# Kernel tuning notes

Measured on AMD Instinct MI355X. Metric: run time of the kernel, lower is better.

The kernel has to match this reference:

```python
import jax, jax.numpy as jnp
import numpy as np

DIM = 4096
NUM_EXPERTS = 8
TOP_K = 2
TOKENS = 8192  # batch 2 * seq 4096


def setup_inputs() -> dict:
    key = jax.random.key(0)
    k1, k2 = jax.random.split(key)
    x = jax.random.normal(k1, (TOKENS, DIM), dtype=jnp.float32)
    W = jax.random.normal(k2, (NUM_EXPERTS, DIM), dtype=jnp.float32) * 0.02  # router weight, trunc-normal-ish
    return {"x": x, "W": W}


def reference(x, W):
    # Routing: linear -> top-k -> softmax over the k selected scores (fp32) -> cast back
    expert_scores = jnp.einsum("td,ed->te", x, W)                       # [T, E]
    top_scores, selected = jax.lax.top_k(expert_scores, TOP_K)          # [T, K], [T, K]
    top_scores = jax.nn.softmax(top_scores.astype(jnp.float32), axis=-1).astype(x.dtype)

    flat_expert_indices = selected.reshape(-1)                           # [T*K]
    # torch.histc(bins=E, min=0, max=E) on integer expert ids == bincount
    num_tokens_per_expert = jnp.bincount(flat_expert_indices, length=NUM_EXPERTS)

    # Stable argsort groups tokens by destination expert, preserving token order within an expert
    sorted_indices = jnp.argsort(flat_expert_indices, stable=True)       # [T*K]
    scatter_indices = sorted_indices // TOP_K                            # original token id per slot
    x_gathered = x[scatter_indices]                                      # [T*K, D]
    scores_sorted = top_scores.reshape(-1)[sorted_indices]               # [T*K]
    return x_gathered, num_tokens_per_expert, scatter_indices, scores_sorted
```

## Files before the change

kernel.cpp:

```cpp
#include <hip/hip_runtime.h>
#include <hip/hip_bf16.h>
#include <cstdint>

#define TOKENS 8192
#define DIM 4096
#define D4 (DIM / 4)
#define NEXP 8
#define TOPK 2
#define SLOTS (TOKENS * TOPK)
#define NCHUNK (SLOTS / 64)

#define OUT_X 0
#define OUT_CNT ((size_t)TOKENS * TOPK * DIM)
#define OUT_SCAT (OUT_CNT + NEXP)
#define OUT_SCORE (OUT_SCAT + SLOTS)

__global__ __launch_bounds__(256) void k_score(const float* __restrict__ x,
                                               const float* __restrict__ W,
                                               int* __restrict__ eid,
                                               float* __restrict__ prob)
{
    const int wave = threadIdx.x >> 6;
    const int lane = threadIdx.x & 63;
    const int tok0 = (blockIdx.x * 4 + wave) * 8;

    const float4* x4 = reinterpret_cast<const float4*>(x);
    const float4* W4 = reinterpret_cast<const float4*>(W);

    float acc[8][NEXP];
#pragma unroll
    for (int t = 0; t < 8; ++t)
#pragma unroll
        for (int e = 0; e < NEXP; ++e) acc[t][e] = 0.f;

    for (int i = 0; i < 16; ++i) {
        const int d4 = lane + 64 * i;
        float4 w[NEXP];
#pragma unroll
        for (int e = 0; e < NEXP; ++e) w[e] = W4[e * D4 + d4];
#pragma unroll
        for (int t = 0; t < 8; ++t) {
            const float4 xv = x4[(size_t)(tok0 + t) * D4 + d4];
#pragma unroll
            for (int e = 0; e < NEXP; ++e) {
                acc[t][e] = fmaf(xv.x, w[e].x, acc[t][e]);
                acc[t][e] = fmaf(xv.y, w[e].y, acc[t][e]);
                acc[t][e] = fmaf(xv.z, w[e].z, acc[t][e]);
                acc[t][e] = fmaf(xv.w, w[e].w, acc[t][e]);
            }
        }
    }

#pragma unroll
    for (int t = 0; t < 8; ++t)
#pragma unroll
        for (int e = 0; e < NEXP; ++e) {
            float v = acc[t][e];
#pragma unroll
            for (int off = 32; off >= 1; off >>= 1) v += __shfl_xor(v, off);
            acc[t][e] = v;
        }

#pragma unroll
    for (int t = 0; t < 8; ++t) {
        int i0 = 0;
        float m0 = acc[t][0];
#pragma unroll
        for (int e = 1; e < NEXP; ++e)
            if (acc[t][e] > m0) { m0 = acc[t][e]; i0 = e; }
        int i1 = -1;
        float m1 = -INFINITY;
#pragma unroll
        for (int e = 0; e < NEXP; ++e)
            if (e != i0 && acc[t][e] > m1) { m1 = acc[t][e]; i1 = e; }
        const float z = __expf(m1 - m0);
        const float inv = 1.0f / (1.0f + z);
        if (lane == t) {
            const int s2 = (tok0 + t) * 2;
            eid[s2] = i0;
            eid[s2 + 1] = i1;
            prob[s2] = inv;
            prob[s2 + 1] = z * inv;
        }
    }
}

__global__ __launch_bounds__(1024) void k_sort(const int* __restrict__ eid,
                                               const float* __restrict__ prob,
                                               int* __restrict__ dstpos,
                                               float* __restrict__ out)
{
    __shared__ int hist[NCHUNK][NEXP];
    const int tid = threadIdx.x;
    const int wave = tid >> 6;
    const int lane = tid & 63;

    for (int c = wave; c < NCHUNK; c += 16) {
        const int s = c * 64 + lane;
        const int e = eid[s];
#pragma unroll
        for (int q = 0; q < NEXP; ++q) {
            const unsigned long long m = __ballot(e == q);
            if (lane == q) hist[c][q] = __popcll(m);
        }
    }
    __syncthreads();

    if (wave == 0) {
        int run[NEXP];
#pragma unroll
        for (int q = 0; q < NEXP; ++q) run[q] = 0;

        for (int r = 0; r < 4; ++r) {
            const int c = r * 64 + lane;
#pragma unroll
            for (int q = 0; q < NEXP; ++q) {
                const int v = hist[c][q];
                int incl = v;
#pragma unroll
                for (int off = 1; off <= 32; off <<= 1) {
                    const int n = __shfl_up(incl, off);
                    if (lane >= off) incl += n;
                }
                hist[c][q] = run[q] + incl - v;
                run[q] += __shfl(incl, 63);
            }
        }
        int eoff[NEXP];
        int a = 0;
#pragma unroll
        for (int q = 0; q < NEXP; ++q) { eoff[q] = a; a += run[q]; }
        for (int r = 0; r < 4; ++r) {
            const int c = r * 64 + lane;
#pragma unroll
            for (int q = 0; q < NEXP; ++q) hist[c][q] += eoff[q];
        }
        if (lane == 0) {
#pragma unroll
            for (int q = 0; q < NEXP; ++q) out[OUT_CNT + q] = (float)run[q];
        }
    }
    __syncthreads();

    for (int c = wave; c < NCHUNK; c += 16) {
        const int s = c * 64 + lane;
        const int e = eid[s];
        const unsigned long long lt = (1ull << lane) - 1ull;
        int rank = 0;
#pragma unroll
        for (int q = 0; q < NEXP; ++q) {
            const unsigned long long m = __ballot(e == q);
            if (e == q) rank = __popcll(m & lt);
        }
        const int p = hist[c][e] + rank;
        dstpos[s] = p;
        out[OUT_SCAT + p] = (float)(s >> 1);
        out[OUT_SCORE + p] = prob[s];
    }
}

__global__ __launch_bounds__(256) void k_gather(const float* __restrict__ x,
                                                const int* __restrict__ dstpos,
                                                float* __restrict__ out)
{
    const int t = blockIdx.x;
    const int p0 = dstpos[t * 2];
    const int p1 = dstpos[t * 2 + 1];
    const float4* x4 = reinterpret_cast<const float4*>(x) + (size_t)t * D4;
    float4* o4 = reinterpret_cast<float4*>(out);
#pragma unroll
    for (int i = 0; i < 4; ++i) {
        const int idx = threadIdx.x + 256 * i;
        const float4 v = x4[idx];
        o4[(size_t)p0 * D4 + idx] = v;
        o4[(size_t)p1 * D4 + idx] = v;
    }
}

extern "C" void kernel_launch(void* const* d_in, const int* in_sizes, int n_in,
                              void* d_out, int out_size, void* d_ws, size_t ws_size,
                              hipStream_t stream)
{
    const float* x = (const float*)d_in[0];
    const float* W = (const float*)d_in[1];
    float* out = (float*)d_out;

    int* eid = (int*)d_ws;
    float* prob = (float*)((char*)d_ws + 64 * 1024);
    int* dstpos = (int*)((char*)d_ws + 128 * 1024);

    k_score<<<TOKENS / 32, 256, 0, stream>>>(x, W, eid, prob);
    k_sort<<<1, 1024, 0, stream>>>(eid, prob, dstpos, out);
    k_gather<<<TOKENS, 256, 0, stream>>>(x, dstpos, out);
}
```

Baseline: 444.9 us.

## Split single-block sort into multi-block hist/scan/pos kernels, retile scoring, nontemporal gather stores

Replaces the single 1024-thread sort kernel with three kernels: a per-chunk histogram across 256 blocks, a one-wave scan, and a per-chunk position/scatter pass across 256 blocks. This spreads the serial sort across the GPU. The scoring kernel drops from 8 to 4 tokens per wave and reorders its loops to load x first, which doubles the block count and lowers register pressure. The gather kernel now uses nontemporal stores for the large output so it does not pollute cache, at the cost of two extra kernel launches.

```diff
diff --git a/kernel.cpp b/kernel.cpp
--- a/kernel.cpp
+++ b/kernel.cpp
@@ -10,10 +10,11 @@
 #define SLOTS (TOKENS * TOPK)
 #define NCHUNK (SLOTS / 64)
 
-#define OUT_X 0
 #define OUT_CNT ((size_t)TOKENS * TOPK * DIM)
 #define OUT_SCAT (OUT_CNT + NEXP)
 #define OUT_SCORE (OUT_SCAT + SLOTS)
+
+typedef float vfloat4 __attribute__((ext_vector_type(4)));
 
 __global__ __launch_bounds__(256) void k_score(const float* __restrict__ x,
                                                const float* __restrict__ W,
@@ -22,37 +23,37 @@
 {
     const int wave = threadIdx.x >> 6;
     const int lane = threadIdx.x & 63;
-    const int tok0 = (blockIdx.x * 4 + wave) * 8;
+    const int tok0 = (blockIdx.x * 4 + wave) * 4;
 
     const float4* x4 = reinterpret_cast<const float4*>(x);
     const float4* W4 = reinterpret_cast<const float4*>(W);
 
-    float acc[8][NEXP];
-#pragma unroll
-    for (int t = 0; t < 8; ++t)
+    float acc[4][NEXP];
+#pragma unroll
+    for (int t = 0; t < 4; ++t)
 #pragma unroll
         for (int e = 0; e < NEXP; ++e) acc[t][e] = 0.f;
 
     for (int i = 0; i < 16; ++i) {
         const int d4 = lane + 64 * i;
-        float4 w[NEXP];
-#pragma unroll
-        for (int e = 0; e < NEXP; ++e) w[e] = W4[e * D4 + d4];
-#pragma unroll
-        for (int t = 0; t < 8; ++t) {
-            const float4 xv = x4[(size_t)(tok0 + t) * D4 + d4];
-#pragma unroll
-            for (int e = 0; e < NEXP; ++e) {
-                acc[t][e] = fmaf(xv.x, w[e].x, acc[t][e]);
-                acc[t][e] = fmaf(xv.y, w[e].y, acc[t][e]);
-                acc[t][e] = fmaf(xv.z, w[e].z, acc[t][e]);
-                acc[t][e] = fmaf(xv.w, w[e].w, acc[t][e]);
+        float4 xv[4];
+#pragma unroll
+        for (int t = 0; t < 4; ++t) xv[t] = x4[(size_t)(tok0 + t) * D4 + d4];
+#pragma unroll
+        for (int e = 0; e < NEXP; ++e) {
+            const float4 w = W4[e * D4 + d4];
+#pragma unroll
+            for (int t = 0; t < 4; ++t) {
+                acc[t][e] = fmaf(xv[t].x, w.x, acc[t][e]);
+                acc[t][e] = fmaf(xv[t].y, w.y, acc[t][e]);
+                acc[t][e] = fmaf(xv[t].z, w.z, acc[t][e]);
+                acc[t][e] = fmaf(xv[t].w, w.w, acc[t][e]);
             }
         }
     }
 
 #pragma unroll
-    for (int t = 0; t < 8; ++t)
+    for (int t = 0; t < 4; ++t)
 #pragma unroll
         for (int e = 0; e < NEXP; ++e) {
             float v = acc[t][e];
@@ -62,7 +63,7 @@
         }
 
 #pragma unroll
-    for (int t = 0; t < 8; ++t) {
+    for (int t = 0; t < 4; ++t) {
         int i0 = 0;
         float m0 = acc[t][0];
 #pragma unroll
@@ -85,78 +86,79 @@
     }
 }
 
-__global__ __launch_bounds__(1024) void k_sort(const int* __restrict__ eid,
-                                               const float* __restrict__ prob,
-                                               int* __restrict__ dstpos,
-                                               float* __restrict__ out)
-{
-    __shared__ int hist[NCHUNK][NEXP];
-    const int tid = threadIdx.x;
-    const int wave = tid >> 6;
-    const int lane = tid & 63;
-
-    for (int c = wave; c < NCHUNK; c += 16) {
-        const int s = c * 64 + lane;
-        const int e = eid[s];
+__global__ __launch_bounds__(64) void k_hist(const int* __restrict__ eid,
+                                             int* __restrict__ hist)
+{
+    const int c = blockIdx.x;
+    const int lane = threadIdx.x;
+    const int e = eid[c * 64 + lane];
+#pragma unroll
+    for (int q = 0; q < NEXP; ++q) {
+        const unsigned long long m = __ballot(e == q);
+        if (lane == q) hist[c * NEXP + q] = __popcll(m);
+    }
+}
+
+__global__ __launch_bounds__(64) void k_scan(int* __restrict__ hist,
+                                             float* __restrict__ out)
+{
+    const int lane = threadIdx.x;
+    int run[NEXP];
+#pragma unroll
+    for (int q = 0; q < NEXP; ++q) run[q] = 0;
+
+    int excl[4][NEXP];
+    for (int r = 0; r < 4; ++r) {
+        const int c = r * 64 + lane;
 #pragma unroll
         for (int q = 0; q < NEXP; ++q) {
-            const unsigned long long m = __ballot(e == q);
-            if (lane == q) hist[c][q] = __popcll(m);
-        }
-    }
-    __syncthreads();
-
-    if (wave == 0) {
-        int run[NEXP];
-#pragma unroll
-        for (int q = 0; q < NEXP; ++q) run[q] = 0;
-
-        for (int r = 0; r < 4; ++r) {
-            const int c = r * 64 + lane;
-#pragma unroll
-            for (int q = 0; q < NEXP; ++q) {
-                const int v = hist[c][q];
-                int incl = v;
-#pragma unroll
-                for (int off = 1; off <= 32; off <<= 1) {
-                    const int n = __shfl_up(incl, off);
-                    if (lane >= off) incl += n;
-                }
-                hist[c][q] = run[q] + incl - v;
-                run[q] += __shfl(incl, 63);
+            const int v = hist[c * NEXP + q];
+            int incl = v;
+#pragma unroll
+            for (int off = 1; off <= 32; off <<= 1) {
+                const int n = __shfl_up(incl, off);
+                if (lane >= off) incl += n;
             }
-        }
-        int eoff[NEXP];
-        int a = 0;
-#pragma unroll
-        for (int q = 0; q < NEXP; ++q) { eoff[q] = a; a += run[q]; }
-        for (int r = 0; r < 4; ++r) {
-            const int c = r * 64 + lane;
-#pragma unroll
-            for (int q = 0; q < NEXP; ++q) hist[c][q] += eoff[q];
-        }
-        if (lane == 0) {
-#pragma unroll
-            for (int q = 0; q < NEXP; ++q) out[OUT_CNT + q] = (float)run[q];
-        }
-    }
-    __syncthreads();
-
-    for (int c = wave; c < NCHUNK; c += 16) {
-        const int s = c * 64 + lane;
-        const int e = eid[s];
-        const unsigned long long lt = (1ull << lane) - 1ull;
-        int rank = 0;
-#pragma unroll
-        for (int q = 0; q < NEXP; ++q) {
-            const unsigned long long m = __ballot(e == q);
-            if (e == q) rank = __popcll(m & lt);
-        }
-        const int p = hist[c][e] + rank;
-        dstpos[s] = p;
-        out[OUT_SCAT + p] = (float)(s >> 1);
-        out[OUT_SCORE + p] = prob[s];
-    }
+            excl[r][q] = run[q] + incl - v;
+            run[q] += __shfl(incl, 63);
+        }
+    }
+    int eoff[NEXP];
+    int a = 0;
+#pragma unroll
+    for (int q = 0; q < NEXP; ++q) { eoff[q] = a; a += run[q]; }
+    for (int r = 0; r < 4; ++r) {
+        const int c = r * 64 + lane;
+#pragma unroll
+        for (int q = 0; q < NEXP; ++q) hist[c * NEXP + q] = excl[r][q] + eoff[q];
+    }
+    if (lane == 0) {
+#pragma unroll
+        for (int q = 0; q < NEXP; ++q) out[OUT_CNT + q] = (float)run[q];
+    }
+}
+
+__global__ __launch_bounds__(64) void k_pos(const int* __restrict__ eid,
+                                            const float* __restrict__ prob,
+                                            const int* __restrict__ hist,
+                                            int* __restrict__ dstpos,
+                                            float* __restrict__ out)
+{
+    const int c = blockIdx.x;
+    const int lane = threadIdx.x;
+    const int s = c * 64 + lane;
+    const int e = eid[s];
+    const unsigned long long lt = (1ull << lane) - 1ull;
+    int rank = 0;
+#pragma unroll
+    for (int q = 0; q < NEXP; ++q) {
+        const unsigned long long m = __ballot(e == q);
+        if (e == q) rank = __popcll(m & lt);
+    }
+    const int p = hist[c * NEXP + e] + rank;
+    dstpos[s] = p;
+    out[OUT_SCAT + p] = (float)(s >> 1);
+    out[OUT_SCORE + p] = prob[s];
 }
 
 __global__ __launch_bounds__(256) void k_gather(const float* __restrict__ x,
@@ -166,14 +168,14 @@
     const int t = blockIdx.x;
     const int p0 = dstpos[t * 2];
     const int p1 = dstpos[t * 2 + 1];
-    const float4* x4 = reinterpret_cast<const float4*>(x) + (size_t)t * D4;
-    float4* o4 = reinterpret_cast<float4*>(out);
+    const vfloat4* x4 = reinterpret_cast<const vfloat4*>(x) + (size_t)t * D4;
+    vfloat4* o4 = reinterpret_cast<vfloat4*>(out);
 #pragma unroll
     for (int i = 0; i < 4; ++i) {
         const int idx = threadIdx.x + 256 * i;
-        const float4 v = x4[idx];
-        o4[(size_t)p0 * D4 + idx] = v;
-        o4[(size_t)p1 * D4 + idx] = v;
+        const vfloat4 v = x4[idx];
+        __builtin_nontemporal_store(v, &o4[(size_t)p0 * D4 + idx]);
+        __builtin_nontemporal_store(v, &o4[(size_t)p1 * D4 + idx]);
     }
 }
 
@@ -188,8 +190,11 @@
     int* eid = (int*)d_ws;
     float* prob = (float*)((char*)d_ws + 64 * 1024);
     int* dstpos = (int*)((char*)d_ws + 128 * 1024);
-
-    k_score<<<TOKENS / 32, 256, 0, stream>>>(x, W, eid, prob);
-    k_sort<<<1, 1024, 0, stream>>>(eid, prob, dstpos, out);
+    int* hist = (int*)((char*)d_ws + 192 * 1024);
+
+    k_score<<<TOKENS / 16, 256, 0, stream>>>(x, W, eid, prob);
+    k_hist<<<NCHUNK, 64, 0, stream>>>(eid, hist);
+    k_scan<<<1, 64, 0, stream>>>(hist, out);
+    k_pos<<<NCHUNK, 64, 0, stream>>>(eid, prob, hist, dstpos, out);
     k_gather<<<TOKENS, 256, 0, stream>>>(x, dstpos, out);
 }
```

After: 389.0 us. -12.6%, faster.
